# Kernel tuning notes

Hardware: AMD Instinct MI355X
Metric: run time of the kernel (lower is better)

## Reference

```python
import jax, jax.numpy as jnp
import numpy as np
from jax import lax

NUM_CLASSES = 2
IOU_THRESH = 0.5
SCORE_THRESH = 0.5
K_CAND = 512        # per-class candidate pool fed to greedy NMS
MAX_PER_CLASS = 100
MAX_TOTAL = 100


def setup_inputs() -> dict:
    key = jax.random.key(0)
    k1, k2, k3 = jax.random.split(key, 3)
    B = 64
    pred_s1 = jax.random.normal(k1, (B, 19, 19, 3, 5 + NUM_CLASSES), dtype=jnp.float32)
    pred_s2 = jax.random.normal(k2, (B, 38, 38, 3, 5 + NUM_CLASSES), dtype=jnp.float32)
    pred_s3 = jax.random.normal(k3, (B, 76, 76, 3, 5 + NUM_CLASSES), dtype=jnp.float32)
    # standard YOLOv3 anchors (pixels) normalized by input size 608
    anchors_px = np.array([[10, 13], [16, 30], [33, 23], [30, 61], [62, 45],
                           [59, 119], [116, 90], [156, 198], [373, 326]], np.float32)
    anchors = jnp.asarray(anchors_px / 608.0)
    return {"pred_s1": pred_s1, "pred_s2": pred_s2, "pred_s3": pred_s3, "anchors": anchors}


def _decode(pred, anch):
    # pred: [B, g, g, A, 5+C]; anch: [A, 2] normalized wh
    g = pred.shape[1]
    box_xy = jax.nn.sigmoid(pred[..., 0:2])
    box_wh = jnp.exp(pred[..., 2:4]) * anch          # broadcast [A,2]
    obj = jax.nn.sigmoid(pred[..., 4:5])
    cls = jax.nn.sigmoid(pred[..., 5:])
    gx, gy = jnp.meshgrid(jnp.arange(g), jnp.arange(g))   # 'xy' indexing, as tf.meshgrid
    grid = jnp.stack([gx, gy], axis=-1)[:, :, None, :].astype(pred.dtype)  # [g,g,1,2]
    xy = (box_xy + grid) / jnp.float32(g)
    x1y1 = xy - box_wh / 2.0
    x2y2 = x1y1 + box_wh                              # YoloNMS: wh + xy(top-left)
    boxes = jnp.concatenate([x1y1, x2y2], axis=-1)    # [B,g,g,A,4]
    scores = obj * cls                                # [B,g,g,A,C]
    B = pred.shape[0]
    return boxes.reshape(B, -1, 4), scores.reshape(B, -1, NUM_CLASSES)


def _pairwise_iou(b):
    # b: [K,4] in (x1,y1,x2,y2); returns [K,K]
    a = b[:, None, :]
    c = b[None, :, :]
    iw = jnp.clip(jnp.minimum(a[..., 2], c[..., 2]) - jnp.maximum(a[..., 0], c[..., 0]), 0.0)
    ih = jnp.clip(jnp.minimum(a[..., 3], c[..., 3]) - jnp.maximum(a[..., 1], c[..., 1]), 0.0)
    inter = iw * ih
    area = jnp.clip(b[:, 2] - b[:, 0], 0.0) * jnp.clip(b[:, 3] - b[:, 1], 0.0)
    union = area[:, None] + area[None, :] - inter
    return inter / jnp.maximum(union, 1e-9)


def _nms_one_class(boxes, scores):
    # boxes: [N,4], scores: [N] -> candidate boxes/scores/keep mask, each len K_CAND
    sc, idx = lax.top_k(scores, K_CAND)               # sorted descending
    bx = boxes[idx]
    iou = lax.stop_gradient(_pairwise_iou(bx))
    valid = sc > SCORE_THRESH
    def body(i, keep):
        suppressed = jnp.any(keep & (iou[i] > IOU_THRESH))
        return keep.at[i].set(valid[i] & ~suppressed)
    keep = lax.fori_loop(0, K_CAND, body, jnp.zeros((K_CAND,), jnp.bool_))
    keep = keep & (jnp.cumsum(keep) <= MAX_PER_CLASS)
    return bx, sc, keep


def _nms_one_image(boxes, scores):
    # boxes: [N,4], scores: [N,C]
    bk, sk, keep = jax.vmap(_nms_one_class, in_axes=(None, 1))(boxes, scores)  # [C,K,*]
    sm = jnp.where(keep, sk, -1.0)
    cls_ids = jnp.broadcast_to(jnp.arange(NUM_CLASSES)[:, None], (NUM_CLASSES, K_CAND))
    sf = sm.reshape(-1)
    bf = bk.reshape(-1, 4)
    cf = cls_ids.reshape(-1)
    ts, ti = lax.top_k(sf, MAX_TOTAL)
    kept = ts > 0.0
    out_boxes = jnp.where(kept[:, None], jnp.clip(bf[ti], 0.0, 1.0), 0.0)  # clip_boxes=True
    out_scores = jnp.where(kept, ts, 0.0)
    out_classes = jnp.where(kept, cf[ti].astype(jnp.float32), 0.0)
    return out_boxes, out_scores, out_classes, jnp.sum(kept).astype(jnp.int32)


def reference(pred_s1, pred_s2, pred_s3, anchors):
    # scale masks: grid19 -> anchors[6:9], grid38 -> anchors[3:6], grid76 -> anchors[0:3]
    b1, s1 = _decode(pred_s1, anchors[6:9])
    b2, s2 = _decode(pred_s2, anchors[3:6])
    b3, s3 = _decode(pred_s3, anchors[0:3])
    boxes = jnp.concatenate([b1, b2, b3], axis=1)     # [B,N,4]
    scores = jnp.concatenate([s1, s2, s3], axis=1)    # [B,N,C]
    return jax.vmap(_nms_one_image)(boxes, scores)
```

## Files before the change

kernel.cpp:

```cpp
#include <hip/hip_runtime.h>
#include <cstdint>
#include <cstddef>

#define NTOT   22743
#define N1     1083
#define N12    5415
#define BATCH  64
#define KCAND  512
#define NSEG   16
#define SEGLEN 1422
#define CAPS   384
#define CAP    4096
#define MAXPC  100
#define MAXTOT 100
#define KITER  6

__device__ __forceinline__ float sigmoidf(float x) { return 1.0f / (1.0f + expf(-x)); }
__device__ __forceinline__ int SK4(int j) { return j + ((j >> 6) << 2); }

__global__ __launch_bounds__(256) void score_filter_kernel(
    const float* __restrict__ p1, const float* __restrict__ p2,
    const float* __restrict__ p3, uint2* __restrict__ cand,
    uint32_t* __restrict__ counts)
{
  const int blk  = blockIdx.x;
  const int b    = blk >> 4;
  const int s    = blk & 15;
  const int tid  = threadIdx.x;
  const int lane = tid & 63;

  __shared__ uint2    lst[2][CAPS];
  __shared__ uint32_t lcnt[2];

  if (tid < 2) lcnt[tid] = 0u;
  __syncthreads();

  const int beg = s * SEGLEN;
  const int end = (beg + SEGLEN < NTOT) ? beg + SEGLEN : NTOT;

  float4 v[KITER];
  #pragma unroll
  for (int k = 0; k < KITER; ++k) {
    int i0 = beg + tid + k * 256;
    if (i0 < end) {
      const float* p; int local, per;
      if (i0 < N1)       { p = p1; local = i0;        per = 1083; }
      else if (i0 < N12) { p = p2; local = i0 - N1;   per = 4332; }
      else               { p = p3; local = i0 - N12;  per = 17328; }
      const float* q = p + ((size_t)b * per + local) * 7;
      v[k] = *(const float4*)(q + 3);
    } else {
      v[k] = make_float4(0.f, -1.f, 0.f, 0.f);
    }
  }

  #pragma unroll
  for (int k = 0; k < KITER; ++k) {
    int i0 = beg + tid + k * 256;
    float s0 = 0.f, s1 = 0.f;
    float q4 = v[k].y;
    if (q4 > 0.f) {
      float obj = sigmoidf(q4);
      s0 = obj * sigmoidf(v[k].z);
      s1 = obj * sigmoidf(v[k].w);
    }
    #pragma unroll
    for (int c = 0; c < 2; c++) {
      float sc = (c == 0) ? s0 : s1;
      bool pred = sc > 0.5f;
      unsigned long long m = __ballot(pred ? 1 : 0);
      if (m != 0ull) {
        int leader = (int)__ffsll(m) - 1;
        uint32_t base = 0u;
        if (lane == leader) base = atomicAdd(&lcnt[c], (uint32_t)__popcll(m));
        base = (uint32_t)__shfl((int)base, leader);
        if (pred) {
          uint32_t off = base + (uint32_t)__popcll(m & ((1ull << lane) - 1ull));
          if (off < CAPS) lst[c][off] = make_uint2(__float_as_uint(sc), (uint32_t)i0);
        }
      }
    }
  }
  __syncthreads();

  #pragma unroll
  for (int c = 0; c < 2; c++) {
    uint32_t cnt = lcnt[c]; if (cnt > CAPS) cnt = CAPS;
    uint2* dst = cand + ((size_t)((b * 2 + c) * NSEG + s)) * CAPS;
    for (uint32_t i = tid; i < cnt; i += 256) dst[i] = lst[c][i];
    if (tid == 0) counts[(b * 2 + c) * NSEG + s] = cnt;
  }
}

__device__ void decode_box(const float* __restrict__ p1, const float* __restrict__ p2,
                           const float* __restrict__ p3, const float* __restrict__ anch,
                           int b, int i, float bb[4])
{
  const float* p; int local, g, abase, per;
  if (i < N1)       { p = p1; local = i;       g = 19; abase = 6; per = 1083; }
  else if (i < N12) { p = p2; local = i - N1;  g = 38; abase = 3; per = 4332; }
  else              { p = p3; local = i - N12; g = 76; abase = 0; per = 17328; }
  const float* q = p + ((size_t)b * per + local) * 7;
  int a    = local % 3;
  int cell = local / 3;
  int col  = cell % g;
  int row  = cell / g;
  float aw = anch[(abase + a) * 2 + 0];
  float ah = anch[(abase + a) * 2 + 1];
  float x = (sigmoidf(q[0]) + (float)col) / (float)g;
  float y = (sigmoidf(q[1]) + (float)row) / (float)g;
  float w = expf(q[2]) * aw;
  float h = expf(q[3]) * ah;
  float x1 = x - w * 0.5f;
  float y1 = y - h * 0.5f;
  bb[0] = x1; bb[1] = y1; bb[2] = x1 + w; bb[3] = y1 + h;
}

__global__ __launch_bounds__(1024) void nms_kernel(
    const uint2* __restrict__ cand, const uint32_t* __restrict__ counts,
    const float* __restrict__ p1, const float* __restrict__ p2,
    const float* __restrict__ p3, const float* __restrict__ anch,
    float* __restrict__ selScore, float* __restrict__ selBox,
    int* __restrict__ selRank, int* __restrict__ selCount)
{
  const int bc   = blockIdx.x;
  const int b    = bc >> 1;
  const int tid  = threadIdx.x;
  const int lane = tid & 63;

  __shared__ __attribute__((aligned(16))) unsigned long long sw[1024];
  __shared__ __attribute__((aligned(16))) float bx1[544];
  __shared__ __attribute__((aligned(16))) float by1[544];
  __shared__ __attribute__((aligned(16))) float bx2[544];
  __shared__ __attribute__((aligned(16))) float by2[544];
  __shared__ __attribute__((aligned(16))) float ar[544];
  __shared__ uint32_t           skey[512];
  __shared__ unsigned long long msk[128][9];
  __shared__ unsigned long long kword[8];
  __shared__ uint32_t           hist3[768];
  __shared__ uint32_t           svar[8];

  if (tid < 768) hist3[tid] = 0u;
  sw[tid] = 0ull;
  if (tid == 0) { svar[0] = 0x3F000000u; svar[2] = KCAND; svar[4] = 0u; svar[5] = 0u; }
  if (tid < 512) {
    skey[tid] = 0u; int p = SK4(tid);
    bx1[p] = 0.f; by1[p] = 0.f; bx2[p] = 0.f; by2[p] = 0.f; ar[p] = 0.f;
  }

  uint32_t pc[17];
  pc[0] = 0;
  #pragma unroll
  for (int t = 0; t < 16; ++t) {
    uint32_t c = counts[bc * NSEG + t];
    if (c > CAPS) c = CAPS;
    pc[t + 1] = pc[t] + c;
  }
  const int n = ((int)pc[16] < CAP) ? (int)pc[16] : CAP;

  unsigned long long v0 = 0ull, v1 = 0ull, v2 = 0ull, v3 = 0ull;
  auto loadc = [&](int i) -> unsigned long long {
    if (i >= n) return 0ull;
    uint32_t ps = 0; int s = 0;
    #pragma unroll
    for (int t = 1; t < 16; ++t) {
      bool ge = (uint32_t)i >= pc[t];
      s += (int)ge; ps = ge ? pc[t] : ps;
    }
    uint2 e = cand[(size_t)(bc * NSEG + s) * CAPS + (i - (int)ps)];
    return ((unsigned long long)e.x << 32) | (uint32_t)(~e.y);
  };
  v0 = loadc(tid); v1 = loadc(tid + 1024); v2 = loadc(tid + 2048); v3 = loadc(tid + 3072);
  __syncthreads();

  uint32_t K = 0u;
  if (n > KCAND) {
    #pragma unroll
    for (int p = 0; p < 3; p++) {
      const int shift = 16 - 8 * p;
      const uint32_t maskB = (p == 0) ? 0xFF000000u : (p == 1) ? 0xFFFF0000u : 0xFFFFFF00u;
      uint32_t* hist = &hist3[p * 256];
      const uint32_t prefix = svar[0];
      {
        uint32_t k;
        k = (uint32_t)(v0 >> 32); if (v0 && (k & maskB) == prefix) atomicAdd(&hist[(k >> shift) & 255u], 1u);
        k = (uint32_t)(v1 >> 32); if (v1 && (k & maskB) == prefix) atomicAdd(&hist[(k >> shift) & 255u], 1u);
        k = (uint32_t)(v2 >> 32); if (v2 && (k & maskB) == prefix) atomicAdd(&hist[(k >> shift) & 255u], 1u);
        k = (uint32_t)(v3 >> 32); if (v3 && (k & maskB) == prefix) atomicAdd(&hist[(k >> shift) & 255u], 1u);
      }
      __syncthreads();
      if (tid < 64) {
        uint32_t h0 = hist[lane * 4 + 0], h1 = hist[lane * 4 + 1];
        uint32_t h2 = hist[lane * 4 + 2], h3 = hist[lane * 4 + 3];
        uint32_t s3 = h3, s2 = h2 + s3, s1 = h1 + s2, s0 = h0 + s1;
        uint32_t acc = s0;
        #pragma unroll
        for (int o = 1; o < 64; o <<= 1) {
          uint32_t v = __shfl_down(acc, (unsigned)o);
          acc += (lane + o < 64) ? v : 0u;
        }
        uint32_t above = acc - s0;
        uint32_t S0 = above + s0, S1 = above + s1, S2 = above + s2, S3 = above + s3, S4 = above;
        uint32_t nd = svar[2];
        if (S0 >= nd && S1 < nd) { svar[0] = prefix | ((uint32_t)(lane * 4 + 0) << shift); svar[2] = nd - S1; }
        if (S1 >= nd && S2 < nd) { svar[0] = prefix | ((uint32_t)(lane * 4 + 1) << shift); svar[2] = nd - S2; }
        if (S2 >= nd && S3 < nd) { svar[0] = prefix | ((uint32_t)(lane * 4 + 2) << shift); svar[2] = nd - S3; }
        if (S3 >= nd && S4 < nd) { svar[0] = prefix | ((uint32_t)(lane * 4 + 3) << shift); svar[2] = nd - S4; }
      }
      __syncthreads();
    }
    K = svar[0];
  }

  {
    auto coll = [&](unsigned long long vv) {
      bool pred = (vv != 0ull) && ((uint32_t)(vv >> 32) >= K);
      unsigned long long m = __ballot(pred ? 1 : 0);
      if (m != 0ull) {
        int leader = (int)__ffsll(m) - 1;
        uint32_t base = 0u;
        if (lane == leader) base = atomicAdd(&svar[4], (uint32_t)__popcll(m));
        base = (uint32_t)__shfl((int)base, leader);
        if (pred) {
          uint32_t q = base + (uint32_t)__popcll(m & ((1ull << lane) - 1ull));
          if (q < 1024u) sw[q] = vv;
        }
      }
    };
    coll(v0); coll(v1); coll(v2); coll(v3);
  }
  __syncthreads();
  const int mc = ((int)svar[4] < 1024) ? (int)svar[4] : 1024;
  const int limit = (n < KCAND) ? n : KCAND;

  if (tid < 256) {
    const ulonglong2* sw2 = (const ulonglong2*)sw;
    const int np = (mc + 1) >> 1;
    unsigned long long E0 = sw[tid], E1 = sw[tid + 256];
    int R0 = 0, R1 = 0;
    auto scat = [&](unsigned long long E, int R) {
      if (E != 0ull && R < KCAND) {
        int idx = (int)(~(uint32_t)E);
        float bb[4];
        decode_box(p1, p2, p3, anch, b, idx, bb);
        int p = SK4(R);
        bx1[p] = bb[0]; by1[p] = bb[1]; bx2[p] = bb[2]; by2[p] = bb[3];
        ar[p]  = fmaxf(bb[2] - bb[0], 0.f) * fmaxf(bb[3] - bb[1], 0.f);
        skey[R] = (uint32_t)(E >> 32);
      }
    };
    if (mc <= 512) {
      for (int j = 0; j < np; ++j) {
        ulonglong2 v = sw2[j];
        R0 += (int)(v.x > E0) + (int)(v.y > E0);
        R1 += (int)(v.x > E1) + (int)(v.y > E1);
      }
      scat(E0, R0); scat(E1, R1);
    } else {
      unsigned long long E2 = sw[tid + 512], E3 = sw[tid + 768];
      int R2 = 0, R3 = 0;
      for (int j = 0; j < np; ++j) {
        ulonglong2 v = sw2[j];
        R0 += (int)(v.x > E0) + (int)(v.y > E0);
        R1 += (int)(v.x > E1) + (int)(v.y > E1);
        R2 += (int)(v.x > E2) + (int)(v.y > E2);
        R3 += (int)(v.x > E3) + (int)(v.y > E3);
      }
      scat(E0, R0); scat(E1, R1); scat(E2, R2); scat(E3, R3);
    }
  }
  __syncthreads();

  unsigned long long Kw = 0ull;
  int kept = 0;
  const int r = tid & 127;
  const int w = tid >> 7;

  for (int ch = 0; ch < 4; ++ch) {
    const int base = ch * 128;
    int rows = limit - base; if (rows > 128) rows = 128;

    if (r < rows) {
      const int i = base + r;
      if (w <= (i >> 6)) {
        const int ip = SK4(i);
        const float x1i = bx1[ip], y1i = by1[ip], x2i = bx2[ip], y2i = by2[ip];
        const float ai = ar[ip];
        unsigned long long mrow = 0ull;
        #pragma unroll
        for (int m4 = 0; m4 < 16; ++m4) {
          const int j0 = (w << 6) + (m4 << 2);
          const int a  = j0 + (w << 2);
          float4 X1 = *(const float4*)&bx1[a];
          float4 Y1 = *(const float4*)&by1[a];
          float4 X2 = *(const float4*)&bx2[a];
          float4 Y2 = *(const float4*)&by2[a];
          float4 AR = *(const float4*)&ar[a];
          #define IOU_BIT(JX1,JY1,JX2,JY2,JAR,J)                              \
            { float iw = fminf(x2i,(JX2)) - fmaxf(x1i,(JX1));                 \
              float ih = fminf(y2i,(JY2)) - fmaxf(y1i,(JY1));                 \
              iw = fmaxf(iw,0.f); ih = fmaxf(ih,0.f);                        \
              float inter = iw*ih;                                            \
              float uni = fmaxf(ai + (JAR) - inter, 1e-9f);                   \
              if ((inter/uni > 0.5f) && ((J) < i))                            \
                mrow |= 1ull << ((J) & 63); }
          IOU_BIT(X1.x, Y1.x, X2.x, Y2.x, AR.x, j0 + 0)
          IOU_BIT(X1.y, Y1.y, X2.y, Y2.y, AR.y, j0 + 1)
          IOU_BIT(X1.z, Y1.z, X2.z, Y2.z, AR.z, j0 + 2)
          IOU_BIT(X1.w, Y1.w, X2.w, Y2.w, AR.w, j0 + 3)
          #undef IOU_BIT
        }
        msk[r][w] = mrow;
      } else {
        msk[r][w] = 0ull;
      }
    }
    __syncthreads();

    if (tid < 64) {
      bool stop = false;
      for (int g = 0; g < 16 && !stop; ++g) {
        int r0 = g * 8;
        if (r0 >= rows) break;
        unsigned long long wbuf[8];
        #pragma unroll
        for (int k2 = 0; k2 < 8; ++k2)
          wbuf[k2] = (lane < 8 && (r0 + k2) < rows) ? msk[r0 + k2][lane] : 0ull;
        #pragma unroll
        for (int k2 = 0; k2 < 8; ++k2) {
          if (!stop) {
            int rr = r0 + k2;
            if (rr >= rows) { stop = true; }
            else {
              int i = base + rr;
              bool ov = (Kw & wbuf[k2]) != 0ull;
              if (!__any(ov)) {
                if (lane == (i >> 6)) Kw |= 1ull << (i & 63);
                if (++kept >= MAXPC) stop = true;
              }
            }
          }
        }
      }
      if (lane == 0) svar[5] = (kept >= MAXPC || (base + (rows > 0 ? rows : 0)) >= limit) ? 1u : 0u;
    }
    __syncthreads();
    if (svar[5] != 0u) break;
  }

  if (tid < 8) kword[tid] = Kw;
  __syncthreads();

  if (tid < 512) {
    int rr = tid;
    int wr = rr >> 6;
    unsigned long long kw = kword[wr];
    if ((kw >> (rr & 63)) & 1ull) {
      uint32_t p = 0;
      for (int ww = 0; ww < wr; ++ww) p += (uint32_t)__popcll(kword[ww]);
      p += (uint32_t)__popcll(kw & ((1ull << (rr & 63)) - 1ull));
      selScore[bc * MAXPC + p] = __uint_as_float(skey[rr]);
      selRank[bc * MAXPC + p]  = rr;
      int rp = SK4(rr);
      float* o = &selBox[(size_t)(bc * MAXPC + p) * 4];
      o[0] = bx1[rp]; o[1] = by1[rp]; o[2] = bx2[rp]; o[3] = by2[rp];
    }
  }
  if (tid == 0) {
    uint32_t tot = 0;
    for (int ww = 0; ww < 8; ++ww) tot += (uint32_t)__popcll(kword[ww]);
    selCount[bc] = (int)tot;
  }
}

__global__ __launch_bounds__(256) void merge_kernel(
    const float* __restrict__ selScore, const float* __restrict__ selBox,
    const int* __restrict__ selRank, const int* __restrict__ selCount,
    float* __restrict__ out)
{
  const int b   = blockIdx.x;
  const int tid = threadIdx.x;
  __shared__ float    es[200];
  __shared__ uint32_t ek[200];
  __shared__ float    eb[200][4];
  const int c0  = selCount[b * 2 + 0];
  const int c1  = selCount[b * 2 + 1];
  const int tot = c0 + c1;

  if (tid < tot) {
    int cls  = (tid < c0) ? 0 : 1;
    int slot = (cls == 0) ? tid : (tid - c0);
    int src  = (b * 2 + cls) * MAXPC + slot;
    es[tid] = selScore[src];
    ek[tid] = (uint32_t)(cls * KCAND + selRank[src]);
    eb[tid][0] = selBox[(size_t)src * 4 + 0];
    eb[tid][1] = selBox[(size_t)src * 4 + 1];
    eb[tid][2] = selBox[(size_t)src * 4 + 2];
    eb[tid][3] = selBox[(size_t)src * 4 + 3];
  }
  __syncthreads();

  float* outBoxes  = out;
  float* outScores = out + (size_t)BATCH * MAXTOT * 4;
  float* outCls    = outScores + (size_t)BATCH * MAXTOT;
  float* outCnt    = outCls + (size_t)BATCH * MAXTOT;
  const int filled = (tot < MAXTOT) ? tot : MAXTOT;

  if (tid < tot) {
    float    s  = es[tid];
    uint32_t fk = ek[tid];
    int rank = 0;
    for (int j = 0; j < tot; j++)
      rank += (int)((es[j] > s) || (es[j] == s && ek[j] < fk));
    if (rank < MAXTOT) {
      outScores[b * MAXTOT + rank] = s;
      outCls[b * MAXTOT + rank]    = (float)(fk >> 9);
      float* ob = &outBoxes[(size_t)(b * MAXTOT + rank) * 4];
      ob[0] = fminf(fmaxf(eb[tid][0], 0.f), 1.f);
      ob[1] = fminf(fmaxf(eb[tid][1], 0.f), 1.f);
      ob[2] = fminf(fmaxf(eb[tid][2], 0.f), 1.f);
      ob[3] = fminf(fmaxf(eb[tid][3], 0.f), 1.f);
    }
  }
  if (tid >= filled && tid < MAXTOT) {
    outScores[b * MAXTOT + tid] = 0.f;
    outCls[b * MAXTOT + tid]    = 0.f;
    float* ob = &outBoxes[(size_t)(b * MAXTOT + tid) * 4];
    ob[0] = 0.f; ob[1] = 0.f; ob[2] = 0.f; ob[3] = 0.f;
  }
  if (tid == 0) outCnt[b] = (float)filled;
}

extern "C" void kernel_launch(void* const* d_in, const int* in_sizes, int n_in,
                              void* d_out, int out_size, void* d_ws, size_t ws_size,
                              hipStream_t stream)
{
  const float* p1   = (const float*)d_in[0];
  const float* p2   = (const float*)d_in[1];
  const float* p3   = (const float*)d_in[2];
  const float* anch = (const float*)d_in[3];

  uint8_t* ws = (uint8_t*)d_ws;
  uint32_t* counts = (uint32_t*)ws;
  uint2*    cand   = (uint2*)(ws + 16384);
  uint8_t*  wp     = ws + 16384 + (size_t)128 * NSEG * CAPS * 8;
  float*    selScore = (float*)wp;         wp += (size_t)BATCH * 2 * MAXPC * 4;
  float*    selBox   = (float*)wp;         wp += (size_t)BATCH * 2 * MAXPC * 16;
  int*      selRank  = (int*)wp;           wp += (size_t)BATCH * 2 * MAXPC * 4;
  int*      selCount = (int*)wp;

  score_filter_kernel<<<BATCH * NSEG, 256, 0, stream>>>(p1, p2, p3, cand, counts);
  nms_kernel<<<BATCH * 2, 1024, 0, stream>>>(cand, counts, p1, p2, p3, anch,
                                             selScore, selBox, selRank, selCount);
  merge_kernel<<<BATCH, 256, 0, stream>>>(selScore, selBox, selRank, selCount,
                                          (float*)d_out);
}
```

Measured before the change: 63.71 us.

## Fuse merge into NMS kernel via last-block flag and bucket the rank sort

Removes the separate merge kernel launch. The second class block of each image to finish, detected with an atomic counter per image after a threadfence, now performs the cross-class top-k merge inside the NMS kernel. The candidate ranking is also reworked: instead of 256 threads each comparing against all survivors, keys are bucketed by an 8-bit histogram with a wave prefix scan, and each thread ranks only within its own bucket. This saves a launch and quadratic compare work, but adds extra syncs, atomics and a risk of skew when buckets are uneven.

```diff
diff --git a/kernel.cpp b/kernel.cpp
--- a/kernel.cpp
+++ b/kernel.cpp
@@ -21,13 +21,15 @@
 __global__ __launch_bounds__(256) void score_filter_kernel(
     const float* __restrict__ p1, const float* __restrict__ p2,
     const float* __restrict__ p3, uint2* __restrict__ cand,
-    uint32_t* __restrict__ counts)
+    uint32_t* __restrict__ counts, uint32_t* __restrict__ imgflag)
 {
   const int blk  = blockIdx.x;
   const int b    = blk >> 4;
   const int s    = blk & 15;
   const int tid  = threadIdx.x;
   const int lane = tid & 63;
+
+  if (blk == 0 && tid < BATCH) imgflag[tid] = 0u;
 
   __shared__ uint2    lst[2][CAPS];
   __shared__ uint32_t lcnt[2];
@@ -121,7 +123,8 @@
     const float* __restrict__ p1, const float* __restrict__ p2,
     const float* __restrict__ p3, const float* __restrict__ anch,
     float* __restrict__ selScore, float* __restrict__ selBox,
-    int* __restrict__ selRank, int* __restrict__ selCount)
+    int* __restrict__ selRank, int* __restrict__ selCount,
+    uint32_t* __restrict__ imgflag, float* __restrict__ out)
 {
   const int bc   = blockIdx.x;
   const int b    = bc >> 1;
@@ -233,40 +236,50 @@
   const int mc = ((int)svar[4] < 1024) ? (int)svar[4] : 1024;
   const int limit = (n < KCAND) ? n : KCAND;
 
-  if (tid < 256) {
-    const ulonglong2* sw2 = (const ulonglong2*)sw;
-    const int np = (mc + 1) >> 1;
-    unsigned long long E0 = sw[tid], E1 = sw[tid + 256];
-    int R0 = 0, R1 = 0;
-    auto scat = [&](unsigned long long E, int R) {
-      if (E != 0ull && R < KCAND) {
-        int idx = (int)(~(uint32_t)E);
-        float bb[4];
-        decode_box(p1, p2, p3, anch, b, idx, bb);
-        int p = SK4(R);
-        bx1[p] = bb[0]; by1[p] = bb[1]; bx2[p] = bb[2]; by2[p] = bb[3];
-        ar[p]  = fmaxf(bb[2] - bb[0], 0.f) * fmaxf(bb[3] - bb[1], 0.f);
-        skey[R] = (uint32_t)(E >> 32);
-      }
-    };
-    if (mc <= 512) {
-      for (int j = 0; j < np; ++j) {
-        ulonglong2 v = sw2[j];
-        R0 += (int)(v.x > E0) + (int)(v.y > E0);
-        R1 += (int)(v.x > E1) + (int)(v.y > E1);
-      }
-      scat(E0, R0); scat(E1, R1);
-    } else {
-      unsigned long long E2 = sw[tid + 512], E3 = sw[tid + 768];
-      int R2 = 0, R3 = 0;
-      for (int j = 0; j < np; ++j) {
-        ulonglong2 v = sw2[j];
-        R0 += (int)(v.x > E0) + (int)(v.y > E0);
-        R1 += (int)(v.x > E1) + (int)(v.y > E1);
-        R2 += (int)(v.x > E2) + (int)(v.y > E2);
-        R3 += (int)(v.x > E3) + (int)(v.y > E3);
-      }
-      scat(E0, R0); scat(E1, R1); scat(E2, R2); scat(E3, R3);
+  if (tid < 512) hist3[tid] = 0u;
+  __syncthreads();
+  uint32_t* bcnt = hist3;
+  uint32_t* boff = hist3 + 256;
+  uint32_t* bpre = hist3 + 512;
+  unsigned long long e = (tid < mc) ? sw[tid] : 0ull;
+  const uint32_t B = (uint32_t)((e >> 47) & 255u);
+  if (tid < mc) atomicAdd(&bcnt[B], 1u);
+  __syncthreads();
+  if (tid < 64) {
+    uint32_t h0 = bcnt[lane * 4 + 0], h1 = bcnt[lane * 4 + 1];
+    uint32_t h2 = bcnt[lane * 4 + 2], h3 = bcnt[lane * 4 + 3];
+    uint32_t s3 = h3, s2 = h2 + s3, s1 = h1 + s2, s0 = h0 + s1;
+    uint32_t acc = s0;
+    #pragma unroll
+    for (int o = 1; o < 64; o <<= 1) {
+      uint32_t v = __shfl_down(acc, (unsigned)o);
+      acc += (lane + o < 64) ? v : 0u;
+    }
+    uint32_t above = acc - s0;
+    bpre[lane * 4 + 0] = above + s1;
+    bpre[lane * 4 + 1] = above + s2;
+    bpre[lane * 4 + 2] = above + s3;
+    bpre[lane * 4 + 3] = above;
+  }
+  __syncthreads();
+  unsigned long long* bord = (unsigned long long*)msk;
+  if (tid < mc) {
+    uint32_t pos = bpre[B] + atomicAdd(&boff[B], 1u);
+    bord[pos] = e;
+  }
+  __syncthreads();
+  if (tid < mc) {
+    const uint32_t lo = bpre[B], sz = bcnt[B];
+    int rank = (int)lo;
+    for (uint32_t j = lo; j < lo + sz; ++j) rank += (int)(bord[j] > e);
+    if (rank < KCAND) {
+      int idx = (int)(~(uint32_t)e);
+      float bb[4];
+      decode_box(p1, p2, p3, anch, b, idx, bb);
+      int p = SK4(rank);
+      bx1[p] = bb[0]; by1[p] = bb[1]; bx2[p] = bb[2]; by2[p] = bb[3];
+      ar[p]  = fmaxf(bb[2] - bb[0], 0.f) * fmaxf(bb[3] - bb[1], 0.f);
+      skey[rank] = (uint32_t)(e >> 32);
     }
   }
   __syncthreads();
@@ -371,32 +384,33 @@
     for (int ww = 0; ww < 8; ++ww) tot += (uint32_t)__popcll(kword[ww]);
     selCount[bc] = (int)tot;
   }
-}
-
-__global__ __launch_bounds__(256) void merge_kernel(
-    const float* __restrict__ selScore, const float* __restrict__ selBox,
-    const int* __restrict__ selRank, const int* __restrict__ selCount,
-    float* __restrict__ out)
-{
-  const int b   = blockIdx.x;
-  const int tid = threadIdx.x;
-  __shared__ float    es[200];
-  __shared__ uint32_t ek[200];
-  __shared__ float    eb[200][4];
-  const int c0  = selCount[b * 2 + 0];
-  const int c1  = selCount[b * 2 + 1];
-  const int tot = c0 + c1;
+
+  __threadfence();
+  __syncthreads();
+  if (tid == 0) {
+    uint32_t old = atomicAdd(&imgflag[b], 1u);
+    svar[6] = (old == 1u) ? 1u : 0u;
+  }
+  __syncthreads();
+  if (svar[6] == 0u) return;
+
+  float*    es  = (float*)sw;
+  uint32_t* ek  = skey;
+  float*    ebx = (float*)msk;
+  const int cc0 = selCount[b * 2 + 0];
+  const int cc1 = selCount[b * 2 + 1];
+  const int tot = cc0 + cc1;
 
   if (tid < tot) {
-    int cls  = (tid < c0) ? 0 : 1;
-    int slot = (cls == 0) ? tid : (tid - c0);
+    int cls  = (tid < cc0) ? 0 : 1;
+    int slot = (cls == 0) ? tid : (tid - cc0);
     int src  = (b * 2 + cls) * MAXPC + slot;
     es[tid] = selScore[src];
     ek[tid] = (uint32_t)(cls * KCAND + selRank[src]);
-    eb[tid][0] = selBox[(size_t)src * 4 + 0];
-    eb[tid][1] = selBox[(size_t)src * 4 + 1];
-    eb[tid][2] = selBox[(size_t)src * 4 + 2];
-    eb[tid][3] = selBox[(size_t)src * 4 + 3];
+    ebx[tid * 4 + 0] = selBox[(size_t)src * 4 + 0];
+    ebx[tid * 4 + 1] = selBox[(size_t)src * 4 + 1];
+    ebx[tid * 4 + 2] = selBox[(size_t)src * 4 + 2];
+    ebx[tid * 4 + 3] = selBox[(size_t)src * 4 + 3];
   }
   __syncthreads();
 
@@ -416,10 +430,10 @@
       outScores[b * MAXTOT + rank] = s;
       outCls[b * MAXTOT + rank]    = (float)(fk >> 9);
       float* ob = &outBoxes[(size_t)(b * MAXTOT + rank) * 4];
-      ob[0] = fminf(fmaxf(eb[tid][0], 0.f), 1.f);
-      ob[1] = fminf(fmaxf(eb[tid][1], 0.f), 1.f);
-      ob[2] = fminf(fmaxf(eb[tid][2], 0.f), 1.f);
-      ob[3] = fminf(fmaxf(eb[tid][3], 0.f), 1.f);
+      ob[0] = fminf(fmaxf(ebx[tid * 4 + 0], 0.f), 1.f);
+      ob[1] = fminf(fmaxf(ebx[tid * 4 + 1], 0.f), 1.f);
+      ob[2] = fminf(fmaxf(ebx[tid * 4 + 2], 0.f), 1.f);
+      ob[3] = fminf(fmaxf(ebx[tid * 4 + 3], 0.f), 1.f);
     }
   }
   if (tid >= filled && tid < MAXTOT) {
@@ -447,11 +461,11 @@
   float*    selScore = (float*)wp;         wp += (size_t)BATCH * 2 * MAXPC * 4;
   float*    selBox   = (float*)wp;         wp += (size_t)BATCH * 2 * MAXPC * 16;
   int*      selRank  = (int*)wp;           wp += (size_t)BATCH * 2 * MAXPC * 4;
-  int*      selCount = (int*)wp;
-
-  score_filter_kernel<<<BATCH * NSEG, 256, 0, stream>>>(p1, p2, p3, cand, counts);
+  int*      selCount = (int*)wp;           wp += (size_t)BATCH * 2 * 4;
+  uint32_t* imgflag  = (uint32_t*)wp;      wp += (size_t)BATCH * 4;
+
+  score_filter_kernel<<<BATCH * NSEG, 256, 0, stream>>>(p1, p2, p3, cand, counts, imgflag);
   nms_kernel<<<BATCH * 2, 1024, 0, stream>>>(cand, counts, p1, p2, p3, anch,
-                                             selScore, selBox, selRank, selCount);
-  merge_kernel<<<BATCH, 256, 0, stream>>>(selScore, selBox, selRank, selCount,
-                                          (float*)d_out);
+                                             selScore, selBox, selRank, selCount,
+                                             imgflag, (float*)d_out);
 }
```

Result: slower. 87.39 us (+37.2%).
